# Kernel optimization log

Hardware: AMD Instinct MI355X
Metric: run time of the kernel (lower is better)

Reference implementation:

```python
import jax, jax.numpy as jnp
import numpy as np

TOP_K = 2  # hard-coded in MoCo.__init__ (self.top_k = 2)


def setup_inputs() -> dict:
    key = jax.random.key(0)
    k1, k2, k3 = jax.random.split(key, 3)
    B, D, E, O = 16384, 4096, 4, 256  # batch, mlp_dim, num_experts, dim
    v_standard = jax.random.normal(k1, (B, D), dtype=jnp.float32)
    router_w = jax.random.normal(k2, (D, E), dtype=jnp.float32) / np.float32(np.sqrt(D))
    expert_w = jax.random.normal(k3, (E, D, O), dtype=jnp.float32) / np.float32(np.sqrt(D))
    return {"v_standard": v_standard, "router_w": router_w, "expert_w": expert_w}


def reference(v_standard, router_w, expert_w):
    # Router + softmax gating: [B, E]
    routing_logits = v_standard @ router_w
    routing_weights = jax.nn.softmax(routing_logits, axis=-1)

    # Top-k gating, renormalized over the selected experts
    topk_weights, topk_indices = jax.lax.top_k(routing_weights, TOP_K)  # [B, k]
    topk_weights = topk_weights / topk_weights.sum(axis=-1, keepdims=True)

    # Dense all-expert compute (as in the original: every expert runs on every token)
    expert_outputs = jnp.einsum('bd,edo->beo', v_standard, expert_w)  # [B, E, O]

    # Gather the top-k expert outputs and combine with gate weights
    selected = jnp.take_along_axis(expert_outputs, topk_indices[:, :, None], axis=1)  # [B, k, O]
    moe_output = (selected * topk_weights[:, :, None]).sum(axis=1)  # [B, O]
    return moe_output, routing_weights
```

## Files before the change

kernel.cpp:

```cpp
#include <hip/hip_runtime.h>

typedef unsigned short ushort_t;
typedef __attribute__((ext_vector_type(8))) short short8;
typedef __attribute__((ext_vector_type(4))) float floatx4;
typedef __attribute__((ext_vector_type(4))) unsigned int uint4v;

static __device__ __forceinline__ unsigned short f2bf_rn(float f) {
  return (unsigned short)((__float_as_uint(f) + 0x8000u) >> 16);
}
static __device__ __forceinline__ unsigned int packbf(float a, float b) {
  return ((__float_as_uint(a) + 0x8000u) >> 16) |
         ((__float_as_uint(b) + 0x8000u) & 0xFFFF0000u);
}

__global__ __launch_bounds__(256) void k_transpose(const float* __restrict__ We,
                                                   ushort_t* __restrict__ WT) {
  __shared__ float tile[32][33];
  int t = threadIdx.x, tx = t & 31, ty = t >> 5;
  int d0 = blockIdx.x * 32, o0 = blockIdx.y * 32, e = blockIdx.z;
  const float* src = We + (size_t)e * 4096 * 256;
  ushort_t* dst = WT + (size_t)e * 256 * 4096;
#pragma unroll
  for (int r = 0; r < 4; ++r)
    tile[ty + r * 8][tx] = src[(size_t)(d0 + ty + r * 8) * 256 + (o0 + tx)];
  __syncthreads();
#pragma unroll
  for (int r = 0; r < 4; ++r)
    dst[(size_t)(o0 + ty + r * 8) * 4096 + (d0 + tx)] = f2bf_rn(tile[tx][ty + r * 8]);
}

__global__ __launch_bounds__(256) void k_routing(const float* __restrict__ V,
                                                 const float* __restrict__ Wr,
                                                 float* __restrict__ rw_out,
                                                 float* __restrict__ gates) {
  int w = threadIdx.x >> 6, lane = threadIdx.x & 63;
  int b = blockIdx.x * 4 + w;
  const float* vrow = V + (size_t)b * 4096;
  float a0 = 0.f, a1 = 0.f, a2 = 0.f, a3 = 0.f;
#pragma unroll
  for (int j = 0; j < 16; ++j) {
    int d = j * 256 + lane * 4;
    float4 vv = *(const float4*)(vrow + d);
    float vals[4] = {vv.x, vv.y, vv.z, vv.w};
#pragma unroll
    for (int u = 0; u < 4; ++u) {
      float4 ww = *(const float4*)(Wr + (size_t)(d + u) * 4);
      a0 += vals[u] * ww.x;
      a1 += vals[u] * ww.y;
      a2 += vals[u] * ww.z;
      a3 += vals[u] * ww.w;
    }
  }
#pragma unroll
  for (int mask = 1; mask < 64; mask <<= 1) {
    a0 += __shfl_xor(a0, mask, 64);
    a1 += __shfl_xor(a1, mask, 64);
    a2 += __shfl_xor(a2, mask, 64);
    a3 += __shfl_xor(a3, mask, 64);
  }
  float mx = fmaxf(fmaxf(a0, a1), fmaxf(a2, a3));
  float e0 = expf(a0 - mx), e1 = expf(a1 - mx), e2 = expf(a2 - mx), e3 = expf(a3 - mx);
  float s = e0 + e1 + e2 + e3;
  float p[4] = {e0 / s, e1 / s, e2 / s, e3 / s};
  int i1 = 0;
#pragma unroll
  for (int k = 1; k < 4; ++k)
    if (p[k] > p[i1]) i1 = k;
  int i2 = (i1 == 0) ? 1 : 0;
#pragma unroll
  for (int k = 0; k < 4; ++k)
    if (k != i1 && p[k] > p[i2]) i2 = k;
  float gs = p[i1] + p[i2];
  if (lane < 4) {
    rw_out[(size_t)b * 4 + lane] = p[lane];
    float g = (lane == i1 || lane == i2) ? (p[lane] / gs) : 0.f;
    gates[(size_t)b * 4 + lane] = g;
  }
}

#define BM 128
#define BN 64
#define BK 64

__global__ __launch_bounds__(256, 2) void k_gemm_moe(const float* __restrict__ V,
                                                     const ushort_t* __restrict__ WT,
                                                     const float* __restrict__ gates,
                                                     float* __restrict__ out) {
  const int Kd = 4096;
  int bn = blockIdx.x;
  int bm = blockIdx.y;
  int m0 = bm * BM, n0 = bn * BN;

  __shared__ __align__(16) ushort_t Asm[BM * BK];
  __shared__ __align__(16) ushort_t Bsm[4 * BN * BK];

  int t = threadIdx.x;
  int w = t >> 6, lane = t & 63;
  int quad = lane >> 4, mi = lane & 15;
  int wm = (w >> 1) * 64, wn = (w & 1) * 32;

  int aG[4], aL[4];
#pragma unroll
  for (int j = 0; j < 4; ++j) {
    int q = j * 256 + t;
    int row = q >> 3, c = q & 7;
    aG[j] = (m0 + row) * Kd + c * 8;
    aL[j] = (row * 8 + (c ^ (row & 7))) * 8;
  }
  int bG[8], bL[8];
#pragma unroll
  for (int j = 0; j < 8; ++j) {
    int q = j * 256 + t;
    int eb = q >> 9, rc = q & 511;
    int r = rc >> 3, c = rc & 7;
    bG[j] = eb * (256 * Kd) + (n0 + r) * Kd + c * 8;
    bL[j] = eb * (BN * BK) + (r * 8 + (c ^ (r & 7))) * 8;
  }

  int aOff[2][4], bOff[2][2];
#pragma unroll
  for (int k32 = 0; k32 < 2; ++k32) {
    int cc = k32 * 4 + quad;
#pragma unroll
    for (int i = 0; i < 4; ++i) {
      int rowa = wm + i * 16 + mi;
      aOff[k32][i] = (rowa * 8 + (cc ^ (rowa & 7))) * 8;
    }
#pragma unroll
    for (int j = 0; j < 2; ++j) {
      int rowb = wn + j * 16 + mi;
      bOff[k32][j] = (rowb * 8 + (cc ^ (rowb & 7))) * 8;
    }
  }

  floatx4 zero = {0.f, 0.f, 0.f, 0.f};
  floatx4 acc[4][4][2];
#pragma unroll
  for (int e = 0; e < 4; ++e)
#pragma unroll
    for (int i = 0; i < 4; ++i)
#pragma unroll
      for (int j = 0; j < 2; ++j) acc[e][i][j] = zero;

  for (int kt = 0; kt < Kd / BK; ++kt) {
    int k0 = kt * BK;
#pragma unroll
    for (int j = 0; j < 4; ++j) {
      const float* ap = V + (size_t)(aG[j] + k0);
      float4 x = *(const float4*)ap;
      float4 y = *(const float4*)(ap + 4);
      uint4v uv;
      uv.x = packbf(x.x, x.y);
      uv.y = packbf(x.z, x.w);
      uv.z = packbf(y.x, y.y);
      uv.w = packbf(y.z, y.w);
      *(uint4v*)(Asm + aL[j]) = uv;
    }
#pragma unroll
    for (int j = 0; j < 8; ++j)
      *(short8*)(Bsm + bL[j]) = *(const short8*)(WT + (size_t)(bG[j] + k0));
    __syncthreads();
#pragma unroll
    for (int k32 = 0; k32 < 2; ++k32) {
      short8 af[4];
#pragma unroll
      for (int i = 0; i < 4; ++i) af[i] = *(const short8*)(Asm + aOff[k32][i]);
#pragma unroll
      for (int e = 0; e < 4; ++e) {
        short8 bfr[2];
#pragma unroll
        for (int j = 0; j < 2; ++j)
          bfr[j] = *(const short8*)(Bsm + e * (BN * BK) + bOff[k32][j]);
#pragma unroll
        for (int i = 0; i < 4; ++i)
#pragma unroll
          for (int j = 0; j < 2; ++j)
            acc[e][i][j] =
                __builtin_amdgcn_mfma_f32_16x16x32_bf16(af[i], bfr[j], acc[e][i][j], 0, 0, 0);
      }
    }
    __syncthreads();
  }

#pragma unroll
  for (int i = 0; i < 4; ++i) {
#pragma unroll
    for (int r = 0; r < 4; ++r) {
      int m = m0 + wm + i * 16 + quad * 4 + r;
      float4 gv = *(const float4*)(gates + (size_t)m * 4);
#pragma unroll
      for (int j = 0; j < 2; ++j) {
        float sv = gv.x * acc[0][i][j][r] + gv.y * acc[1][i][j][r] +
                   gv.z * acc[2][i][j][r] + gv.w * acc[3][i][j][r];
        out[(size_t)m * 256 + n0 + wn + j * 16 + mi] = sv;
      }
    }
  }
}

extern "C" void kernel_launch(void* const* d_in, const int* in_sizes, int n_in,
                              void* d_out, int out_size, void* d_ws, size_t ws_size,
                              hipStream_t stream) {
  const float* V = (const float*)d_in[0];
  const float* Wr = (const float*)d_in[1];
  const float* We = (const float*)d_in[2];

  float* out_moe = (float*)d_out;
  float* out_rw = out_moe + (size_t)16384 * 256;

  char* ws = (char*)d_ws;
  float* gates = (float*)ws;
  ushort_t* WT = (ushort_t*)(ws + 262144);

  k_transpose<<<dim3(128, 8, 4), 256, 0, stream>>>(We, WT);
  k_routing<<<dim3(4096), 256, 0, stream>>>(V, Wr, out_rw, gates);
  k_gemm_moe<<<dim3(4, 128), 256, 0, stream>>>(V, WT, gates, out_moe);
}
```

Measured before the change: 616.0 us.

## Prefetch next GEMM tile into registers and transpose router weights for coalesced loads

The GEMM main loop now loads the next K-tile of V and WT into registers right after the barrier, so those global loads overlap the MFMA work on the current tile. It keeps one register-staged prefetch buffer instead of loading and converting inside the same iteration. Separately, a small kernel transposes the router weights into four contiguous per-expert rows, so each routing thread reads float4 vectors instead of four strided float4 loads. Prefetching adds register pressure, which could hurt occupancy under the 2-blocks launch bound, and the extra launch adds a little overhead.

```diff
diff --git a/kernel.cpp b/kernel.cpp
--- a/kernel.cpp
+++ b/kernel.cpp
@@ -29,8 +29,18 @@
     dst[(size_t)(o0 + ty + r * 8) * 4096 + (d0 + tx)] = f2bf_rn(tile[tx][ty + r * 8]);
 }
 
+__global__ __launch_bounds__(256) void k_prep_router(const float* __restrict__ Wr,
+                                                     float* __restrict__ WrT32) {
+  int d = blockIdx.x * 256 + threadIdx.x;
+  float4 w = *(const float4*)(Wr + (size_t)d * 4);
+  WrT32[d] = w.x;
+  WrT32[4096 + d] = w.y;
+  WrT32[2 * 4096 + d] = w.z;
+  WrT32[3 * 4096 + d] = w.w;
+}
+
 __global__ __launch_bounds__(256) void k_routing(const float* __restrict__ V,
-                                                 const float* __restrict__ Wr,
+                                                 const float* __restrict__ WrT32,
                                                  float* __restrict__ rw_out,
                                                  float* __restrict__ gates) {
   int w = threadIdx.x >> 6, lane = threadIdx.x & 63;
@@ -41,15 +51,14 @@
   for (int j = 0; j < 16; ++j) {
     int d = j * 256 + lane * 4;
     float4 vv = *(const float4*)(vrow + d);
-    float vals[4] = {vv.x, vv.y, vv.z, vv.w};
-#pragma unroll
-    for (int u = 0; u < 4; ++u) {
-      float4 ww = *(const float4*)(Wr + (size_t)(d + u) * 4);
-      a0 += vals[u] * ww.x;
-      a1 += vals[u] * ww.y;
-      a2 += vals[u] * ww.z;
-      a3 += vals[u] * ww.w;
-    }
+    float4 w0 = *(const float4*)(WrT32 + d);
+    float4 w1 = *(const float4*)(WrT32 + 4096 + d);
+    float4 w2 = *(const float4*)(WrT32 + 2 * 4096 + d);
+    float4 w3 = *(const float4*)(WrT32 + 3 * 4096 + d);
+    a0 += vv.x * w0.x + vv.y * w0.y + vv.z * w0.z + vv.w * w0.w;
+    a1 += vv.x * w1.x + vv.y * w1.y + vv.z * w1.z + vv.w * w1.w;
+    a2 += vv.x * w2.x + vv.y * w2.y + vv.z * w2.z + vv.w * w2.w;
+    a3 += vv.x * w3.x + vv.y * w3.y + vv.z * w3.z + vv.w * w3.w;
   }
 #pragma unroll
   for (int mask = 1; mask < 64; mask <<= 1) {
@@ -73,8 +82,7 @@
   float gs = p[i1] + p[i2];
   if (lane < 4) {
     rw_out[(size_t)b * 4 + lane] = p[lane];
-    float g = (lane == i1 || lane == i2) ? (p[lane] / gs) : 0.f;
-    gates[(size_t)b * 4 + lane] = g;
+    gates[(size_t)b * 4 + lane] = (lane == i1 || lane == i2) ? (p[lane] / gs) : 0.f;
   }
 }
 
@@ -142,24 +150,43 @@
 #pragma unroll
       for (int j = 0; j < 2; ++j) acc[e][i][j] = zero;
 
+  float4 ax[4], ay[4];
+  short8 bv[8];
+#pragma unroll
+  for (int j = 0; j < 4; ++j) {
+    const float* ap = V + (size_t)aG[j];
+    ax[j] = *(const float4*)ap;
+    ay[j] = *(const float4*)(ap + 4);
+  }
+#pragma unroll
+  for (int j = 0; j < 8; ++j) bv[j] = *(const short8*)(WT + (size_t)bG[j]);
+
   for (int kt = 0; kt < Kd / BK; ++kt) {
-    int k0 = kt * BK;
 #pragma unroll
     for (int j = 0; j < 4; ++j) {
-      const float* ap = V + (size_t)(aG[j] + k0);
-      float4 x = *(const float4*)ap;
-      float4 y = *(const float4*)(ap + 4);
       uint4v uv;
-      uv.x = packbf(x.x, x.y);
-      uv.y = packbf(x.z, x.w);
-      uv.z = packbf(y.x, y.y);
-      uv.w = packbf(y.z, y.w);
+      uv.x = packbf(ax[j].x, ax[j].y);
+      uv.y = packbf(ax[j].z, ax[j].w);
+      uv.z = packbf(ay[j].x, ay[j].y);
+      uv.w = packbf(ay[j].z, ay[j].w);
       *(uint4v*)(Asm + aL[j]) = uv;
     }
 #pragma unroll
-    for (int j = 0; j < 8; ++j)
-      *(short8*)(Bsm + bL[j]) = *(const short8*)(WT + (size_t)(bG[j] + k0));
+    for (int j = 0; j < 8; ++j) *(short8*)(Bsm + bL[j]) = bv[j];
     __syncthreads();
+
+    if (kt + 1 < Kd / BK) {
+      int k0n = (kt + 1) * BK;
+#pragma unroll
+      for (int j = 0; j < 4; ++j) {
+        const float* ap = V + (size_t)(aG[j] + k0n);
+        ax[j] = *(const float4*)ap;
+        ay[j] = *(const float4*)(ap + 4);
+      }
+#pragma unroll
+      for (int j = 0; j < 8; ++j) bv[j] = *(const short8*)(WT + (size_t)(bG[j] + k0n));
+    }
+
 #pragma unroll
     for (int k32 = 0; k32 < 2; ++k32) {
       short8 af[4];
@@ -211,8 +238,10 @@
   char* ws = (char*)d_ws;
   float* gates = (float*)ws;
   ushort_t* WT = (ushort_t*)(ws + 262144);
+  float* WrT32 = (float*)(ws + 262144 + 8388608);
 
   k_transpose<<<dim3(128, 8, 4), 256, 0, stream>>>(We, WT);
-  k_routing<<<dim3(4096), 256, 0, stream>>>(V, Wr, out_rw, gates);
+  k_prep_router<<<dim3(16), 256, 0, stream>>>(Wr, WrT32);
+  k_routing<<<dim3(4096), 256, 0, stream>>>(V, WrT32, out_rw, gates);
   k_gemm_moe<<<dim3(4, 128), 256, 0, stream>>>(V, WT, gates, out_moe);
 }
```

New measurement: 598.0 us. 2.9% less time.
